# Kernel tuning notes

Hardware: AMD Instinct MI355X
Metric: run time of the kernel (lower is better)

Reference implementation:

```python
import jax, jax.numpy as jnp
import numpy as np

B, N, C, H = 64, 198, 768, 12
D = C // H  # head_dim = 64


def lsq_binary(x, alpha):
    """Elastic (LSQ-style) symmetric binarization with STE: out = alpha*sign(x/alpha)."""
    xs = x / alpha
    return alpha * (xs + jax.lax.stop_gradient(jnp.sign(xs) - xs))


def lsq_bin01(x, alpha):
    """Asymmetric binarization to levels {0, alpha} with STE (for post-softmax attention)."""
    xs = x / alpha
    qh = jnp.clip(jnp.round(xs), 0.0, 1.0)
    return alpha * (xs + jax.lax.stop_gradient(qh - xs))


def gsb(x, alphas, bin_fn):
    """Group-superposition binarization: sum of residual binarizations with per-group scales."""
    out = jnp.zeros_like(x)
    r = x
    for a in alphas:  # fixed small loop over 3 groups
        b = bin_fn(r, a)
        out = out + b
        r = r - b
    return out


def bwn(w):
    """Binary-weight-network weight fake-quant (layerwise scale = mean|w|) with STE."""
    q = jnp.mean(jnp.abs(w)) * jnp.sign(w)
    return w + jax.lax.stop_gradient(q - w)


def setup_inputs() -> dict:
    key = jax.random.key(0)
    ks = jax.random.split(key, 8)
    one = jnp.ones((), jnp.float32)
    return {
        "x": jax.random.normal(ks[0], (B, N, C), jnp.float32),
        "qkv_w": jax.random.normal(ks[1], (3 * C, C), jnp.float32) * 0.02,
        "proj_w": jax.random.normal(ks[2], (C, C), jnp.float32) * 0.02,
        "proj_b": jnp.zeros((C,), jnp.float32),
        "move_q_b": jax.random.normal(ks[3], (H, 1, D), jnp.float32) * 0.01,
        "move_k_b": jax.random.normal(ks[4], (H, 1, D), jnp.float32) * 0.01,
        "move_v_b": jax.random.normal(ks[5], (H, 1, D), jnp.float32) * 0.01,
        "move_att_b": jax.random.normal(ks[6], (H, N, N), jnp.float32) * 0.01,
        "clip_in_qkv": one, "clip_query": one, "clip_key": one,
        "clip_v1": one, "clip_v2": one * 0.5, "clip_v3": one * 0.25,
        "clip_a1": one, "clip_a2": one * 0.5, "clip_a3": one * 0.25,
        "clip_in_proj": one,
    }


def reference(x, qkv_w, proj_w, proj_b, move_q_b, move_k_b, move_v_b, move_att_b,
              clip_in_qkv, clip_query, clip_key, clip_v1, clip_v2, clip_v3,
              clip_a1, clip_a2, clip_a3, clip_in_proj):
    b, n, c = x.shape
    scale = D ** -0.5
    # quantized qkv projection (binary act, BWN weight)
    xq = lsq_binary(x, clip_in_qkv)
    qkv = jnp.einsum('bnc,oc->bno', xq, bwn(qkv_w))  # [B,N,3C]
    qkv = qkv.reshape(b, n, 3, H, D).transpose(2, 0, 3, 1, 4)  # [3,B,H,N,D]
    q, k, v = qkv[0], qkv[1], qkv[2]
    # learnable per-head bias shifts, then fake-quant
    q = lsq_binary(q + move_q_b, clip_query)
    k = lsq_binary(k + move_k_b, clip_key)
    v = gsb(v + move_v_b, (clip_v1, clip_v2, clip_v3), lsq_binary)
    attn = jax.nn.softmax(jnp.einsum('bhnd,bhmd->bhnm', q, k) * scale, axis=-1)
    attn = attn + move_att_b  # [H,N,N] broadcast over batch
    attn = gsb(attn, (clip_a1, clip_a2, clip_a3), lsq_bin01)
    out = jnp.einsum('bhnm,bhmd->bhnd', attn, v).transpose(0, 2, 1, 3).reshape(b, n, c)
    # quantized output projection
    outq = lsq_binary(out, clip_in_proj)
    return jnp.einsum('bnc,oc->bno', outq, bwn(proj_w)) + proj_b
```

## Files before the change

kernel.cpp:

```cpp
#include <hip/hip_runtime.h>
#include <hip/hip_bf16.h>

typedef __attribute__((ext_vector_type(8))) short short8;
typedef __attribute__((ext_vector_type(4))) float f32x4;
typedef __attribute__((ext_vector_type(4))) int int4v;
typedef __attribute__((ext_vector_type(8))) char char8v;
typedef __attribute__((ext_vector_type(4), aligned(4))) unsigned int uint4a;

static constexpr int B = 64, N = 198, C = 768, H = 12, D = 64;
static constexpr int M = B * N;
static constexpr int BH = B * H;
static constexpr int O3C = 3 * C;
static constexpr int KC = 48;
static constexpr int NXT = 198;
static constexpr int NXTP = 200;
static constexpr int AL8 = 272;
static constexpr int VNP = 256;
static constexpr int TLQ = 272;
static constexpr int TLV = 80;


static constexpr size_t OFF_MEANS = 0;
static constexpr size_t OFF_TAB   = 256;
static constexpr size_t OFF_PARTA = 2048;
static constexpr size_t OFF_PARTP = 4096;
static constexpr size_t OFF_XS    = 8192;
static constexpr size_t SZ_XS     = (size_t)M * C;
static constexpr size_t OFF_WQS   = OFF_XS + SZ_XS;
static constexpr size_t SZ_WQS    = (size_t)O3C * C;
static constexpr size_t OFF_WPS   = OFF_WQS + SZ_WQS;
static constexpr size_t SZ_WPS    = (size_t)C * C;
static constexpr size_t OFF_Q     = OFF_WPS + SZ_WPS;
static constexpr size_t SZ_QK8    = (size_t)BH * N * D;
static constexpr size_t OFF_K     = OFF_Q + SZ_QK8;
static constexpr size_t OFF_VT    = OFF_K + SZ_QK8;
static constexpr size_t SZ_VT8    = (size_t)BH * D * VNP;
static constexpr size_t OFF_OS    = OFF_VT + SZ_VT8;

__global__ void reduce_abs2_kernel(const float* __restrict__ qw, int nq,
                                   const float* __restrict__ pw, int np,
                                   double* __restrict__ partA, double* __restrict__ partP) {
  __shared__ double sm[256];
  const float* src;
  int n, b;
  double* dst;
  if (blockIdx.x < 256) { src = qw; n = nq; dst = partA; b = blockIdx.x; }
  else                  { src = pw; n = np; dst = partP; b = blockIdx.x - 256; }
  double s = 0.0;
  for (int i = b * 256 + threadIdx.x; i < n; i += 256 * 256)
    s += (double)fabsf(src[i]);
  sm[threadIdx.x] = s;
  __syncthreads();
  for (int off = 128; off > 0; off >>= 1) {
    if (threadIdx.x < (unsigned)off) sm[threadIdx.x] += sm[threadIdx.x + off];
    __syncthreads();
  }
  if (threadIdx.x == 0) dst[b] = sm[0];
}

__global__ void finalize_kernel(const double* __restrict__ pA, const double* __restrict__ pP,
                                double* __restrict__ means, double* __restrict__ tab,
                                const float* cq, const float* ck) {
  __shared__ double sm[256];
  int t = threadIdx.x;
  sm[t] = pA[t];
  __syncthreads();
  for (int off = 128; off > 0; off >>= 1) { if (t < off) sm[t] += sm[t + off]; __syncthreads(); }
  if (t == 0) means[0] = sm[0] / (double)((size_t)O3C * C);
  __syncthreads();
  sm[t] = pP[t];
  __syncthreads();
  for (int off = 128; off > 0; off >>= 1) { if (t < off) sm[t] += sm[t + off]; __syncthreads(); }
  if (t == 0) means[1] = sm[0] / (double)((size_t)C * C);
  double delta = (double)cq[0] * (double)ck[0] * 0.125;
  if (t < 129) tab[t] = exp((double)(t - 128) * delta);
  if (t < 16) tab[129 + t] = exp((double)t * delta);
}

__global__ void sign8_tiled_kernel(const float* __restrict__ x, signed char* __restrict__ Xs,
                                   const float* __restrict__ qw, signed char* __restrict__ Wq,
                                   const float* __restrict__ pw, signed char* __restrict__ Wp,
                                   int ux, int uq, int up, const float* alpha) {
  float a = alpha[0];
  signed char posx = (a > 0.0f) ? 1 : ((a < 0.0f) ? -1 : 0);
  int total = ux + uq + up;
  int stride = 256 * gridDim.x;
  for (int u = blockIdx.x * 256 + threadIdx.x; u < total; u += stride) {
    const float* src;
    signed char* dst;
    int j;
    signed char pos;
    if (u < ux) { src = x; dst = Xs; j = u; pos = posx; }
    else if (u < ux + uq) { src = qw; dst = Wq; j = u - ux; pos = 1; }
    else { src = pw; dst = Wp; j = u - ux - uq; pos = 1; }
    signed char neg = (signed char)(-pos);
    int row = j / KC, kc = j - row * KC;
    const float4* xp = (const float4*)(src + (size_t)row * C + kc * 16);
    signed char out16[16];
#pragma unroll
    for (int q4 = 0; q4 < 4; ++q4) {
      float4 v = xp[q4];
      float vv[4] = {v.x, v.y, v.z, v.w};
#pragma unroll
      for (int k = 0; k < 4; ++k)
        out16[q4 * 4 + k] = vv[k] > 0.0f ? pos : (vv[k] < 0.0f ? neg : (signed char)0);
    }
    size_t off = (((size_t)(row >> 4) * KC + kc) * 16 + (row & 15)) * 16;
    *(uint4a*)(dst + off) = *(const uint4a*)out16;
  }
}

static __device__ inline bool xcd_decode(int lin, int nyb, int limit, int& x, int& y) {
  int k = lin & 7;
  int q = lin >> 3;
  int xi = q / nyb;
  y = q - xi * nyb;
  x = xi * 8 + k;
  return x < limit;
}

static __device__ inline void gemm_reg_i8(const signed char* __restrict__ At,
                                          const signed char* __restrict__ Bt,
                                          int x4, int nt0, int4v acc[4][4]) {
  int lane = threadIdx.x & 63;
#pragma unroll
  for (int t = 0; t < 12; ++t) {
    int4v af[4], bf[4];
#pragma unroll
    for (int m = 0; m < 4; ++m)
      af[m] = *(const int4v*)&At[((size_t)(x4 + m) * KC + t * 4) * 256 + lane * 16];
#pragma unroll
    for (int n2 = 0; n2 < 4; ++n2)
      bf[n2] = *(const int4v*)&Bt[((size_t)(nt0 + n2) * KC + t * 4) * 256 + lane * 16];
#pragma unroll
    for (int m = 0; m < 4; ++m)
#pragma unroll
      for (int n2 = 0; n2 < 4; ++n2)
        acc[m][n2] = __builtin_amdgcn_mfma_i32_16x16x64_i8(af[m], bf[n2], acc[m][n2], 0, 0, 0);
  }
}

__global__ __launch_bounds__(256) void gemm1_kernel(
    const signed char* __restrict__ Xs, const signed char* __restrict__ Wqs,
    const double* __restrict__ means,
    const float* cin, const float* cq, const float* ck,
    const float* cv1, const float* cv2, const float* cv3,
    const float* __restrict__ movq, const float* __restrict__ movk, const float* __restrict__ movv,
    signed char* __restrict__ Qs8, signed char* __restrict__ Ks8, signed char* __restrict__ Vt8) {
  int bx, by;
  if (!xcd_decode(blockIdx.x, 9, NXT, bx, by)) return;
  __shared__ __align__(16) signed char tile8[20480];
  int tid = threadIdx.x;
  int lane = tid & 63, w = tid >> 6;
  int4v acc[4][4] = {};
  gemm_reg_i8(Xs, Wqs, bx * 4, by * 16 + w * 4, acc);
  double cw_ = (double)cin[0] * means[0];
  float dq = cq[0], dk = ck[0];
  signed char sq8 = dq > 0.0f ? 1 : (dq < 0.0f ? -1 : 0);
  signed char sk8 = dk > 0.0f ? 1 : (dk < 0.0f ? -1 : 0);
  double aa1 = fabs((double)cv1[0]), aa2 = fabs((double)cv2[0]), aa3 = fabs((double)cv3[0]);
  int t = by / 3;
  int rem0 = (by - t * 3) * 256;
  signed char sg8 = t == 0 ? sq8 : sk8;
  const float* mov = t == 0 ? movq : (t == 1 ? movk : movv);
  int g = lane >> 4, q16 = lane & 15;
#pragma unroll
  for (int m = 0; m < 4; ++m)
#pragma unroll
    for (int n2 = 0; n2 < 4; ++n2)
#pragma unroll
      for (int r = 0; r < 4; ++r) {
        int rowL = m * 16 + g * 4 + r;
        int colL = w * 64 + n2 * 16 + q16;
        int rem = rem0 + colL;
        int h = rem >> 6, d = rem & 63;
        double gg = (double)acc[m][n2][r] * cw_;
        if (t < 2) {
          double v = gg + (double)mov[h * D + d];
          tile8[rowL * TLQ + colL] = v > 0.0 ? sg8 : (v < 0.0 ? (signed char)(-sg8) : (signed char)0);
        } else {
          double rr = gg + (double)mov[h * D + d];
          double b1 = rr > 0.0 ? aa1 : (rr < 0.0 ? -aa1 : 0.0);
          rr -= b1;
          double b2 = rr > 0.0 ? aa2 : (rr < 0.0 ? -aa2 : 0.0);
          rr -= b2;
          double b3 = rr > 0.0 ? aa3 : (rr < 0.0 ? -aa3 : 0.0);
          tile8[colL * TLV + rowL] = (signed char)(int)rint(4.0 * (b1 + b2 + b3));
        }
      }
  __syncthreads();
  if (t < 2) {
    signed char* dst = t == 0 ? Qs8 : Ks8;
#pragma unroll
    for (int it = 0; it < 4; ++it) {
      int c = tid + it * 256;
      int rowL = c >> 4, cch = c & 15;
      int gr = bx * 64 + rowL;
      int b = gr / N, nn = gr - b * N;
      int rem = rem0 + cch * 16;
      int h = rem >> 6, d = rem & 63;
      *(uint4a*)&dst[((size_t)(b * H + h) * N + nn) * 64 + d] =
          *(const uint4a*)&tile8[rowL * TLQ + cch * 16];
    }
  } else {
#pragma unroll
    for (int it = 0; it < 4; ++it) {
      int c = tid + it * 256;
      int colL = c >> 2, tch = c & 3;
      int rem = rem0 + colL;
      int h = rem >> 6, d = rem & 63;
      int gr0 = bx * 64 + tch * 16;
      int b0 = gr0 / N, nn0 = gr0 - b0 * N;
      if (nn0 + 16 <= N) {
        *(uint4a*)&Vt8[((size_t)(b0 * H + h) * 64 + d) * VNP + nn0] =
            *(const uint4a*)&tile8[colL * TLV + tch * 16];
      } else {
#pragma unroll
        for (int j = 0; j < 16; ++j) {
          int gr = gr0 + j;
          int b = gr / N, nn = gr - b * N;
          Vt8[((size_t)(b * H + h) * 64 + d) * VNP + nn] = tile8[colL * TLV + tch * 16 + j];
        }
      }
    }
  }
}

__global__ __launch_bounds__(256) void attn_kernel(
    const signed char* __restrict__ Qs8, const signed char* __restrict__ Ks8,
    const signed char* __restrict__ Vt8, const double* __restrict__ tab,
    const float* __restrict__ movatt,
    const float* ca1p, const float* ca2p, const float* ca3p, const float* cipp,
    signed char* __restrict__ Os) {
  __shared__ double Tl1[9];
  __shared__ double Tl2[16];
  __shared__ signed char Al8[4][16 * AL8];
  int i = blockIdx.x;
  int xcd = i & 7;
  int q = i >> 3;
  int rt = q % 13;
  int grp = q / 13;
  int tid = threadIdx.x;
  int w = tid >> 6, lane = tid & 63;
  int bh = (grp * 4 + w) * 8 + xcd;
  int b = bh / H, h = bh - b * H;
  int g = lane >> 4, q16 = lane & 15;
  if (tid < 9) Tl1[tid] = tab[16 * tid];
  if (tid >= 32 && tid < 48) Tl2[tid - 32] = tab[129 + (tid - 32)];
  for (int ii = lane; ii < 192; ii += 64) {
    int row = ii / 12, cd = ii - row * 12;
    *(int*)&Al8[w][row * AL8 + 208 + cd * 4] = 0;
  }
  __syncthreads();
  double ca1 = (double)ca1p[0], ca2 = (double)ca2p[0], ca3 = (double)ca3p[0];
  double t1 = 0.5 * ca1, t2 = 0.5 * ca2, t3 = 0.5 * ca3;
  int q1 = (int)rint(4.0 * ca1), q2 = (int)rint(4.0 * ca2), q3 = (int)rint(4.0 * ca3);
  float cip = cipp[0];
  signed char cp = cip > 0.0f ? 1 : (cip < 0.0f ? -1 : 0);

  int4v qf = {};
  int qrow = rt * 16 + q16;
  if (qrow < N) qf = *(const int4v*)&Qs8[((size_t)bh * N + qrow) * 64 + g * 16];
  int4v sacc[13] = {};
#pragma unroll
  for (int ct = 0; ct < 13; ++ct) {
    int krow = ct * 16 + q16;
    int4v kf = {};
    if (krow < N) kf = *(const int4v*)&Ks8[((size_t)bh * N + krow) * 64 + g * 16];
    sacc[ct] = __builtin_amdgcn_mfma_i32_16x16x64_i8(qf, kf, sacc[ct], 0, 0, 0);
  }
#pragma unroll
  for (int r = 0; r < 4; ++r) {
    int rowg = rt * 16 + g * 4 + r;
    int rowc = rowg < N ? rowg : N - 1;
    const float* mrow = movatt + ((size_t)h * N + rowc) * N;
    int mx = -1000000;
#pragma unroll
    for (int ct = 0; ct < 13; ++ct) {
      int colc = ct * 16 + q16;
      if (colc < N) mx = max(mx, sacc[ct][r]);
    }
    mx = max(mx, __shfl_xor(mx, 1));
    mx = max(mx, __shfl_xor(mx, 2));
    mx = max(mx, __shfl_xor(mx, 4));
    mx = max(mx, __shfl_xor(mx, 8));
    double ev[13];
    double ssum = 0.0;
#pragma unroll
    for (int ct = 0; ct < 13; ++ct) {
      int colc = ct * 16 + q16;
      int idx = sacc[ct][r] - mx + 128;
      idx = idx > 128 ? 128 : idx;
      double e = (colc < N) ? Tl1[idx >> 4] * Tl2[idx & 15] : 0.0;
      ev[ct] = e;
      ssum += e;
    }
    ssum += __shfl_xor(ssum, 1);
    ssum += __shfl_xor(ssum, 2);
    ssum += __shfl_xor(ssum, 4);
    ssum += __shfl_xor(ssum, 8);
    double rec = 1.0 / ssum;
#pragma unroll
    for (int ct = 0; ct < 13; ++ct) {
      int colc = ct * 16 + q16;
      int colb = colc < N ? colc : N - 1;
      double at = ev[ct] * rec + (double)mrow[colb];
      int p4 = 0;
      double rr = at;
      if (rr > t1) { p4 += q1; rr -= ca1; }
      if (rr > t2) { p4 += q2; rr -= ca2; }
      if (rr > t3) { p4 += q3; }
      Al8[w][(g * 4 + r) * AL8 + colc] = (signed char)((colc < N) ? p4 : 0);
    }
  }
  int4v oacc[4] = {};
#pragma unroll
  for (int kt = 0; kt < 4; ++kt) {
    int4v af = *(const int4v*)&Al8[w][q16 * AL8 + kt * 64 + g * 16];
#pragma unroll
    for (int dt = 0; dt < 4; ++dt) {
      int4v bv = *(const int4v*)&Vt8[((size_t)bh * 64 + dt * 16 + q16) * VNP + kt * 64 + g * 16];
      oacc[dt] = __builtin_amdgcn_mfma_i32_16x16x64_i8(af, bv, oacc[dt], 0, 0, 0);
    }
  }
#pragma unroll
  for (int dt = 0; dt < 4; ++dt)
#pragma unroll
    for (int r = 0; r < 4; ++r) {
      int rowg = rt * 16 + g * 4 + r;
      if (rowg < N) {
        size_t grow = (size_t)b * N + rowg;
        int s = oacc[dt][r];
        Os[(grow >> 4) * (KC * 256) + (size_t)(h * 4 + dt) * 256 + (grow & 15) * 16 + q16] =
            s > 0 ? cp : (s < 0 ? (signed char)(-cp) : (signed char)0);
      }
    }
}

__global__ __launch_bounds__(256) void gemm2_kernel(
    const signed char* __restrict__ Ot, const signed char* __restrict__ Wps,
    const double* __restrict__ means, const float* cip, const float* __restrict__ proj_b,
    float* __restrict__ out) {
  int bx, by;
  if (!xcd_decode(blockIdx.x, 3, NXT, bx, by)) return;
  int tid = threadIdx.x;
  int lane = tid & 63, w = tid >> 6;
  int4v acc[4][4] = {};
  gemm_reg_i8(Ot, Wps, bx * 4, by * 16 + w * 4, acc);
  double cw_ = (double)cip[0] * means[1];
  int g = lane >> 4, q16 = lane & 15;
#pragma unroll
  for (int m = 0; m < 4; ++m)
#pragma unroll
    for (int n2 = 0; n2 < 4; ++n2)
#pragma unroll
      for (int r = 0; r < 4; ++r) {
        int row = bx * 64 + m * 16 + g * 4 + r;
        int col = by * 256 + w * 64 + n2 * 16 + q16;
        double v = (double)acc[m][n2][r] * cw_ + (double)proj_b[col];
        out[(size_t)row * C + col] = (float)v;
      }
}

extern "C" void kernel_launch(void* const* d_in, const int* in_sizes, int n_in,
                              void* d_out, int out_size, void* d_ws, size_t ws_size,
                              hipStream_t stream) {
  const float* x      = (const float*)d_in[0];
  const float* qkv_w  = (const float*)d_in[1];
  const float* proj_w = (const float*)d_in[2];
  const float* proj_b = (const float*)d_in[3];
  const float* movq   = (const float*)d_in[4];
  const float* movk   = (const float*)d_in[5];
  const float* movv   = (const float*)d_in[6];
  const float* movatt = (const float*)d_in[7];
  const float* c_inq  = (const float*)d_in[8];
  const float* c_q    = (const float*)d_in[9];
  const float* c_k    = (const float*)d_in[10];
  const float* c_v1   = (const float*)d_in[11];
  const float* c_v2   = (const float*)d_in[12];
  const float* c_v3   = (const float*)d_in[13];
  const float* c_a1   = (const float*)d_in[14];
  const float* c_a2   = (const float*)d_in[15];
  const float* c_a3   = (const float*)d_in[16];
  const float* c_inp  = (const float*)d_in[17];

  char* ws = (char*)d_ws;
  double* means = (double*)(ws + OFF_MEANS);
  double* tab   = (double*)(ws + OFF_TAB);
  double* partA = (double*)(ws + OFF_PARTA);
  double* partP = (double*)(ws + OFF_PARTP);
  signed char* Xs  = (signed char*)(ws + OFF_XS);
  signed char* Wqs = (signed char*)(ws + OFF_WQS);
  signed char* Wps = (signed char*)(ws + OFF_WPS);
  signed char* Qs8 = (signed char*)(ws + OFF_Q);
  signed char* Ks8 = (signed char*)(ws + OFF_K);
  signed char* Vt8 = (signed char*)(ws + OFF_VT);
  signed char* Os  = (signed char*)(ws + OFF_OS);

  reduce_abs2_kernel<<<512, 256, 0, stream>>>(qkv_w, O3C * C, proj_w, C * C, partA, partP);
  finalize_kernel<<<1, 256, 0, stream>>>(partA, partP, means, tab, c_q, c_k);
  sign8_tiled_kernel<<<2048, 256, 0, stream>>>(x, Xs, qkv_w, Wqs, proj_w, Wps,
                                               M * KC, O3C * KC, C * KC, c_inq);
  gemm1_kernel<<<NXTP * 9, 256, 0, stream>>>(
      Xs, Wqs, means, c_inq, c_q, c_k, c_v1, c_v2, c_v3, movq, movk, movv, Qs8, Ks8, Vt8);
  attn_kernel<<<8 * 13 * (BH / 32), 256, 0, stream>>>(Qs8, Ks8, Vt8, tab, movatt, c_a1, c_a2, c_a3, c_inp, Os);
  gemm2_kernel<<<NXTP * 3, 256, 0, stream>>>(
      Os, Wps, means, c_inp, proj_b, (float*)d_out);
}
```

Measured before the change: 174.4 us.

## Fuse weight abs-sum reduction into sign kernel and double-buffer GEMM fragment loads

The separate reduce_abs2 kernel is removed. The sign/packing kernel now also accumulates per-block sums of |w| for both weight matrices in double, and writes 2048 partials each that finalize_kernel then reduces. This drops one launch and a second read of the weights. Separately, the int8 MFMA GEMM inner loop now prefetches the next K-step's A/B fragments into a second register set, so loads overlap with MFMAs at the cost of more VGPRs. The workspace offsets grow to hold the larger partial arrays, and every thread in the sign kernel now does extra double-precision adds.

```diff
diff --git a/kernel.cpp b/kernel.cpp
--- a/kernel.cpp
+++ b/kernel.cpp
@@ -23,8 +23,8 @@
 static constexpr size_t OFF_MEANS = 0;
 static constexpr size_t OFF_TAB   = 256;
 static constexpr size_t OFF_PARTA = 2048;
-static constexpr size_t OFF_PARTP = 4096;
-static constexpr size_t OFF_XS    = 8192;
+static constexpr size_t OFF_PARTP = 18432;
+static constexpr size_t OFF_XS    = 36864;
 static constexpr size_t SZ_XS     = (size_t)M * C;
 static constexpr size_t OFF_WQS   = OFF_XS + SZ_XS;
 static constexpr size_t SZ_WQS    = (size_t)O3C * C;
@@ -37,38 +37,21 @@
 static constexpr size_t SZ_VT8    = (size_t)BH * D * VNP;
 static constexpr size_t OFF_OS    = OFF_VT + SZ_VT8;
 
-__global__ void reduce_abs2_kernel(const float* __restrict__ qw, int nq,
-                                   const float* __restrict__ pw, int np,
-                                   double* __restrict__ partA, double* __restrict__ partP) {
-  __shared__ double sm[256];
-  const float* src;
-  int n, b;
-  double* dst;
-  if (blockIdx.x < 256) { src = qw; n = nq; dst = partA; b = blockIdx.x; }
-  else                  { src = pw; n = np; dst = partP; b = blockIdx.x - 256; }
-  double s = 0.0;
-  for (int i = b * 256 + threadIdx.x; i < n; i += 256 * 256)
-    s += (double)fabsf(src[i]);
-  sm[threadIdx.x] = s;
-  __syncthreads();
-  for (int off = 128; off > 0; off >>= 1) {
-    if (threadIdx.x < (unsigned)off) sm[threadIdx.x] += sm[threadIdx.x + off];
-    __syncthreads();
-  }
-  if (threadIdx.x == 0) dst[b] = sm[0];
-}
-
 __global__ void finalize_kernel(const double* __restrict__ pA, const double* __restrict__ pP,
                                 double* __restrict__ means, double* __restrict__ tab,
                                 const float* cq, const float* ck) {
   __shared__ double sm[256];
   int t = threadIdx.x;
-  sm[t] = pA[t];
+  double s = 0.0;
+  for (int j = t; j < 2048; j += 256) s += pA[j];
+  sm[t] = s;
   __syncthreads();
   for (int off = 128; off > 0; off >>= 1) { if (t < off) sm[t] += sm[t + off]; __syncthreads(); }
   if (t == 0) means[0] = sm[0] / (double)((size_t)O3C * C);
   __syncthreads();
-  sm[t] = pP[t];
+  s = 0.0;
+  for (int j = t; j < 2048; j += 256) s += pP[j];
+  sm[t] = s;
   __syncthreads();
   for (int off = 128; off > 0; off >>= 1) { if (t < off) sm[t] += sm[t + off]; __syncthreads(); }
   if (t == 0) means[1] = sm[0] / (double)((size_t)C * C);
@@ -80,34 +63,58 @@
 __global__ void sign8_tiled_kernel(const float* __restrict__ x, signed char* __restrict__ Xs,
                                    const float* __restrict__ qw, signed char* __restrict__ Wq,
                                    const float* __restrict__ pw, signed char* __restrict__ Wp,
-                                   int ux, int uq, int up, const float* alpha) {
+                                   int ux, int uq, int up, const float* alpha,
+                                   double* __restrict__ partA, double* __restrict__ partP) {
+  __shared__ double sm[256];
   float a = alpha[0];
   signed char posx = (a > 0.0f) ? 1 : ((a < 0.0f) ? -1 : 0);
   int total = ux + uq + up;
   int stride = 256 * gridDim.x;
+  double sq = 0.0, sp = 0.0;
   for (int u = blockIdx.x * 256 + threadIdx.x; u < total; u += stride) {
     const float* src;
     signed char* dst;
     int j;
     signed char pos;
-    if (u < ux) { src = x; dst = Xs; j = u; pos = posx; }
-    else if (u < ux + uq) { src = qw; dst = Wq; j = u - ux; pos = 1; }
-    else { src = pw; dst = Wp; j = u - ux - uq; pos = 1; }
+    int which;
+    if (u < ux) { src = x; dst = Xs; j = u; pos = posx; which = 0; }
+    else if (u < ux + uq) { src = qw; dst = Wq; j = u - ux; pos = 1; which = 1; }
+    else { src = pw; dst = Wp; j = u - ux - uq; pos = 1; which = 2; }
     signed char neg = (signed char)(-pos);
     int row = j / KC, kc = j - row * KC;
     const float4* xp = (const float4*)(src + (size_t)row * C + kc * 16);
     signed char out16[16];
+    double asum = 0.0;
 #pragma unroll
     for (int q4 = 0; q4 < 4; ++q4) {
       float4 v = xp[q4];
       float vv[4] = {v.x, v.y, v.z, v.w};
 #pragma unroll
-      for (int k = 0; k < 4; ++k)
+      for (int k = 0; k < 4; ++k) {
         out16[q4 * 4 + k] = vv[k] > 0.0f ? pos : (vv[k] < 0.0f ? neg : (signed char)0);
-    }
+        asum += (double)fabsf(vv[k]);
+      }
+    }
+    if (which == 1) sq += asum;
+    else if (which == 2) sp += asum;
     size_t off = (((size_t)(row >> 4) * KC + kc) * 16 + (row & 15)) * 16;
     *(uint4a*)(dst + off) = *(const uint4a*)out16;
   }
+  sm[threadIdx.x] = sq;
+  __syncthreads();
+  for (int off = 128; off > 0; off >>= 1) {
+    if (threadIdx.x < (unsigned)off) sm[threadIdx.x] += sm[threadIdx.x + off];
+    __syncthreads();
+  }
+  if (threadIdx.x == 0) partA[blockIdx.x] = sm[0];
+  __syncthreads();
+  sm[threadIdx.x] = sp;
+  __syncthreads();
+  for (int off = 128; off > 0; off >>= 1) {
+    if (threadIdx.x < (unsigned)off) sm[threadIdx.x] += sm[threadIdx.x + off];
+    __syncthreads();
+  }
+  if (threadIdx.x == 0) partP[blockIdx.x] = sm[0];
 }
 
 static __device__ inline bool xcd_decode(int lin, int nyb, int limit, int& x, int& y) {
@@ -123,20 +130,35 @@
                                           const signed char* __restrict__ Bt,
                                           int x4, int nt0, int4v acc[4][4]) {
   int lane = threadIdx.x & 63;
-#pragma unroll
-  for (int t = 0; t < 12; ++t) {
-    int4v af[4], bf[4];
+  const signed char* ap = At + ((size_t)x4 * KC) * 256 + lane * 16;
+  const signed char* bp = Bt + ((size_t)nt0 * KC) * 256 + lane * 16;
+  int4v a0[4], b0[4], a1[4], b1[4];
+#pragma unroll
+  for (int m = 0; m < 4; ++m) a0[m] = *(const int4v*)(ap + (size_t)m * KC * 256);
+#pragma unroll
+  for (int n = 0; n < 4; ++n) b0[n] = *(const int4v*)(bp + (size_t)n * KC * 256);
+#pragma unroll
+  for (int t = 0; t < 12; t += 2) {
+#pragma unroll
+    for (int m = 0; m < 4; ++m) a1[m] = *(const int4v*)(ap + (size_t)m * KC * 256 + (t + 1) * 1024);
+#pragma unroll
+    for (int n = 0; n < 4; ++n) b1[n] = *(const int4v*)(bp + (size_t)n * KC * 256 + (t + 1) * 1024);
 #pragma unroll
     for (int m = 0; m < 4; ++m)
-      af[m] = *(const int4v*)&At[((size_t)(x4 + m) * KC + t * 4) * 256 + lane * 16];
-#pragma unroll
-    for (int n2 = 0; n2 < 4; ++n2)
-      bf[n2] = *(const int4v*)&Bt[((size_t)(nt0 + n2) * KC + t * 4) * 256 + lane * 16];
+#pragma unroll
+      for (int n = 0; n < 4; ++n)
+        acc[m][n] = __builtin_amdgcn_mfma_i32_16x16x64_i8(a0[m], b0[n], acc[m][n], 0, 0, 0);
+    if (t + 2 < 12) {
+#pragma unroll
+      for (int m = 0; m < 4; ++m) a0[m] = *(const int4v*)(ap + (size_t)m * KC * 256 + (t + 2) * 1024);
+#pragma unroll
+      for (int n = 0; n < 4; ++n) b0[n] = *(const int4v*)(bp + (size_t)n * KC * 256 + (t + 2) * 1024);
+    }
 #pragma unroll
     for (int m = 0; m < 4; ++m)
 #pragma unroll
-      for (int n2 = 0; n2 < 4; ++n2)
-        acc[m][n2] = __builtin_amdgcn_mfma_i32_16x16x64_i8(af[m], bf[n2], acc[m][n2], 0, 0, 0);
+      for (int n = 0; n < 4; ++n)
+        acc[m][n] = __builtin_amdgcn_mfma_i32_16x16x64_i8(a1[m], b1[n], acc[m][n], 0, 0, 0);
   }
 }
 
@@ -397,10 +419,10 @@
   signed char* Vt8 = (signed char*)(ws + OFF_VT);
   signed char* Os  = (signed char*)(ws + OFF_OS);
 
-  reduce_abs2_kernel<<<512, 256, 0, stream>>>(qkv_w, O3C * C, proj_w, C * C, partA, partP);
+  sign8_tiled_kernel<<<2048, 256, 0, stream>>>(x, Xs, qkv_w, Wqs, proj_w, Wps,
+                                               M * KC, O3C * KC, C * KC, c_inq,
+                                               partA, partP);
   finalize_kernel<<<1, 256, 0, stream>>>(partA, partP, means, tab, c_q, c_k);
-  sign8_tiled_kernel<<<2048, 256, 0, stream>>>(x, Xs, qkv_w, Wqs, proj_w, Wps,
-                                               M * KC, O3C * KC, C * KC, c_inq);
   gemm1_kernel<<<NXTP * 9, 256, 0, stream>>>(
       Xs, Wqs, means, c_inq, c_q, c_k, c_v1, c_v2, c_v3, movq, movk, movv, Qs8, Ks8, Vt8);
   attn_kernel<<<8 * 13 * (BH / 32), 256, 0, stream>>>(Qs8, Ks8, Vt8, tab, movatt, c_a1, c_a2, c_a3, c_inp, Os);
```

Measured after the change: 187.0 us. 7.2% more time.
